# Kernel optimization log

Hardware: AMD Instinct MI355X
Metric: run time of the kernel (lower is better)

Reference implementation:

```python
import jax, jax.numpy as jnp
import numpy as np

N, F, H, R, E = 50000, 128, 128, 8, 800000
BN_EPS = 1e-5


def setup_inputs() -> dict:
    key = jax.random.key(0)
    ks = jax.random.split(key, 10)
    g = lambda k, shp: jax.random.normal(k, shp, dtype=jnp.float32) * (1.0 / np.sqrt(shp[-2] if len(shp) > 1 else shp[-1]))
    return {
        "x": jax.random.normal(ks[0], (N, F), dtype=jnp.float32),
        "edge_index": jax.random.randint(ks[1], (2, E), 0, N, dtype=jnp.int32),
        "edge_type": jax.random.randint(ks[2], (E,), 0, R, dtype=jnp.int32),
        "W1": g(ks[3], (F, H)),
        "b1": jnp.zeros((H,), jnp.float32),
        "weight": g(ks[4], (R, H, H)),
        "root": g(ks[5], (H, H)),
        "bias_c": jnp.zeros((H,), jnp.float32),
        "gamma": jnp.ones((H,), jnp.float32),
        "beta": jnp.zeros((H,), jnp.float32),
        "W2": g(ks[6], (H, H)),
        "b2": jnp.zeros((H,), jnp.float32),
        "Wo": g(ks[7], (H, 1)),
        "bo": jnp.zeros((1,), jnp.float32),
    }


def reference(x, edge_index, edge_type, W1, b1, weight, root, bias_c, gamma, beta, W2, b2, Wo, bo):
    n = x.shape[0]
    r = weight.shape[0]
    src, dst = edge_index[0], edge_index[1]
    # segment id combining relation and destination node: equivalent to the
    # per-relation edge-mask + scatter-add loop in RGCNConv, but in one pass.
    seg = edge_type.astype(jnp.int32) * n + dst

    def conv(h):
        msg = h[src]                                            # [E, H] gather
        agg = jax.ops.segment_sum(msg, seg, num_segments=r * n)  # [R*N, H]
        agg = agg.reshape(r, n, -1)                             # [R, N, H]
        out = jnp.einsum('rnc,rco->no', agg, weight)            # per-relation matmul, summed
        return out + h @ root + bias_c

    def bn(h):
        mu = h.mean(axis=0)
        var = h.var(axis=0)  # biased var, matches torch BN training normalization
        return gamma * (h - mu) * jax.lax.rsqrt(var + BN_EPS) + beta

    h = x @ W1 + b1
    h = jax.nn.relu(bn(conv(h)))
    h = jax.nn.relu(bn(conv(h)))
    h = h @ W2 + b2
    h = h @ Wo + bo
    return jax.nn.sigmoid(h)
```

## Files before the change

kernel.cpp:

```cpp
#include <hip/hip_runtime.h>
#include <stdint.h>

typedef __bf16 bf16;
typedef __bf16 bf16x8 __attribute__((ext_vector_type(8)));
typedef float f32x4 __attribute__((ext_vector_type(4)));

__device__ __forceinline__ float bfbits2f(uint32_t lo16) {
    uint32_t b = lo16 << 16;
    float f;
    __builtin_memcpy(&f, &b, 4);
    return f;
}

__device__ __forceinline__ void gload_lds16(const void* g, void* l) {
    __builtin_amdgcn_global_load_lds((const __attribute__((address_space(1))) void*)g,
                                     (__attribute__((address_space(3))) void*)l, 16, 0, 0);
}

__global__ void k_prep(const float* __restrict__ W1, const float* __restrict__ weight,
                       const float* __restrict__ root, const float* __restrict__ W2,
                       const float* __restrict__ b2, const float* __restrict__ Wo,
                       const float* __restrict__ bo, bf16* __restrict__ W1T,
                       bf16* __restrict__ WhwT, float* __restrict__ qc, int R) {
    int total = 16384 * (R + 2);
    for (int i = blockIdx.x * blockDim.x + threadIdx.x; i < total + 129; i += gridDim.x * blockDim.x) {
        if (i < 16384) {
            int f = i >> 7, h = i & 127;
            W1T[h * 128 + f] = (bf16)W1[f * 128 + h];
        } else if (i < total) {
            int j = i - 16384;
            int r = j >> 14, rem = j & 16383, c = rem >> 7, k = rem & 127;
            float v = (r < R) ? weight[((size_t)(r * 128 + k)) * 128 + c] : root[(size_t)k * 128 + c];
            WhwT[(size_t)(r * 128 + c) * 128 + k] = (bf16)v;
        } else {
            int t = i - total;
            if (t < 128) {
                float s = 0.f;
                for (int j = 0; j < 128; j++) s += W2[t * 128 + j] * Wo[j];
                qc[t] = s;
            } else {
                float c = bo[0];
                for (int j = 0; j < 128; j++) c += b2[j] * Wo[j];
                qc[128] = c;
            }
        }
    }
}

__global__ void k_hist(const int* __restrict__ dst, int* __restrict__ cnt, int E) {
    for (int e = blockIdx.x * blockDim.x + threadIdx.x; e < E; e += gridDim.x * blockDim.x)
        atomicAdd(&cnt[dst[e]], 1);
}

__global__ __launch_bounds__(256) void k_scan_blk(const int* __restrict__ cnt, int* __restrict__ bsum, int N) {
    int i = blockIdx.x * 256 + threadIdx.x;
    int v = (i < N) ? cnt[i] : 0;
#pragma unroll
    for (int d = 1; d < 64; d <<= 1) v += __shfl_xor(v, d);
    __shared__ int ws[4];
    if ((threadIdx.x & 63) == 0) ws[threadIdx.x >> 6] = v;
    __syncthreads();
    if (threadIdx.x == 0) bsum[blockIdx.x] = ws[0] + ws[1] + ws[2] + ws[3];
}

__global__ __launch_bounds__(256) void k_scan_top(int* __restrict__ bsum, int nb) {
    __shared__ int s[256];
    int t = threadIdx.x;
    int v = (t < nb) ? bsum[t] : 0;
    s[t] = v;
    __syncthreads();
#pragma unroll
    for (int d = 1; d < 256; d <<= 1) {
        int u = (t >= d) ? s[t - d] : 0;
        __syncthreads();
        s[t] += u;
        __syncthreads();
    }
    if (t < nb) bsum[t] = s[t] - v;
}

__global__ __launch_bounds__(256) void k_scan_apply(const int* __restrict__ cnt, const int* __restrict__ bsum,
                                                    int* __restrict__ row_off, int* __restrict__ cursor, int N) {
    int b = blockIdx.x, t = threadIdx.x;
    int i = b * 256 + t;
    int v = (i < N) ? cnt[i] : 0;
    int lane = t & 63, wid = t >> 6;
    int incl = v;
#pragma unroll
    for (int d = 1; d < 64; d <<= 1) {
        int u = __shfl_up(incl, d);
        if (lane >= d) incl += u;
    }
    __shared__ int ws[4];
    if (lane == 63) ws[wid] = incl;
    __syncthreads();
    int woff = 0;
    for (int wj = 0; wj < 4; wj++)
        if (wj < wid) woff += ws[wj];
    int excl = bsum[b] + woff + incl - v;
    if (i < N) {
        row_off[i] = excl;
        cursor[i] = excl;
        if (i == N - 1) row_off[N] = excl + v;
    }
}

__global__ void k_fill(const int* __restrict__ src, const int* __restrict__ dst,
                       const int* __restrict__ etype, int* __restrict__ cursor,
                       int* __restrict__ csr, int E, int pbase) {
    int p = blockIdx.x & 7;
    int bg = blockIdx.x >> 3;
    int nchunk = gridDim.x >> 3;
    int chunk = (E + nchunk - 1) / nchunk;
    int beg = bg * chunk, end = min(beg + chunk, E);
    int lo = p * pbase, hi = lo + pbase;
    for (int e = beg + (int)threadIdx.x; e < end; e += blockDim.x) {
        int d = dst[e];
        if (d >= lo && d < hi) {
            int pos = atomicAdd(&cursor[d], 1);
            csr[pos] = (etype[e] << 16) | src[e];
        }
    }
}

__global__ __launch_bounds__(256) void k_gemm0(const float* __restrict__ A, const bf16* __restrict__ BT,
                                               const float* __restrict__ bias, bf16* __restrict__ C, int M) {
    __shared__ bf16 sA[128 * 128];
    __shared__ bf16 sB[128 * 128];
    int tid = threadIdx.x;
    int m0 = blockIdx.x * 128;
#pragma unroll
    for (int i = 0; i < 8; i++) {
        int chunk = i * 256 + tid;
        int row = chunk >> 4, c16 = chunk & 15;
        int sw = ((c16 ^ (row & 7)) << 3);
        int gr = m0 + row;
        int4 va = {0, 0, 0, 0};
        if (gr < M) {
            const float* ap = A + (size_t)gr * 128 + (c16 << 3);
            float4 f0 = *reinterpret_cast<const float4*>(ap);
            float4 f1 = *reinterpret_cast<const float4*>(ap + 4);
            bf16 tmp[8] = {(bf16)f0.x, (bf16)f0.y, (bf16)f0.z, (bf16)f0.w,
                           (bf16)f1.x, (bf16)f1.y, (bf16)f1.z, (bf16)f1.w};
            __builtin_memcpy(&va, tmp, 16);
        }
        *reinterpret_cast<int4*>(&sA[row * 128 + sw]) = va;
        int4 vb = *reinterpret_cast<const int4*>(&BT[(size_t)row * 128 + (c16 << 3)]);
        *reinterpret_cast<int4*>(&sB[row * 128 + sw]) = vb;
    }
    __syncthreads();

    int lane = tid & 63, w = tid >> 6;
    int wm = (w >> 1) * 64, wn = (w & 1) * 64;
    int lr = lane & 15, lk = lane >> 4;
    f32x4 zero = {0.f, 0.f, 0.f, 0.f};
    f32x4 acc[4][4];
#pragma unroll
    for (int mi = 0; mi < 4; mi++)
#pragma unroll
        for (int ni = 0; ni < 4; ni++) acc[mi][ni] = zero;

#pragma unroll
    for (int kk = 0; kk < 4; kk++) {
        int c = (kk << 2) + lk;
        bf16x8 af[4], bfr[4];
#pragma unroll
        for (int mi = 0; mi < 4; mi++) {
            int r = wm + mi * 16 + lr;
            af[mi] = *reinterpret_cast<const bf16x8*>(&sA[r * 128 + ((c ^ (r & 7)) << 3)]);
        }
#pragma unroll
        for (int ni = 0; ni < 4; ni++) {
            int r = wn + ni * 16 + lr;
            bfr[ni] = *reinterpret_cast<const bf16x8*>(&sB[r * 128 + ((c ^ (r & 7)) << 3)]);
        }
#pragma unroll
        for (int mi = 0; mi < 4; mi++)
#pragma unroll
            for (int ni = 0; ni < 4; ni++)
                acc[mi][ni] = __builtin_amdgcn_mfma_f32_16x16x32_bf16(af[mi], bfr[ni], acc[mi][ni], 0, 0, 0);
    }

#pragma unroll
    for (int ni = 0; ni < 4; ni++) {
        int col = wn + ni * 16 + lr;
        float bia = bias[col];
#pragma unroll
        for (int mi = 0; mi < 4; mi++) {
#pragma unroll
            for (int j = 0; j < 4; j++) {
                int row = m0 + wm + mi * 16 + lk * 4 + j;
                if (row < M) C[(size_t)row * 128 + col] = (bf16)(acc[mi][ni][j] + bia);
            }
        }
    }
}

__global__ __launch_bounds__(256) void k_hwgemm(const bf16* __restrict__ h, const bf16* __restrict__ WhwT,
                                                bf16* __restrict__ HW, int M, int NS) {
    __shared__ bf16 sA[128 * 128];
    __shared__ bf16 sB[128 * 128];
    int tid = threadIdx.x;
    int m0 = blockIdx.x * 128;
    int lane = tid & 63, w = tid >> 6;
    int l4 = lane >> 4, c16 = lane & 15;
    int wm = (w >> 1) * 64, wn = (w & 1) * 64;
    int lr = lane & 15, lk = lane >> 4;
    int ldhw = NS * 128;

#pragma unroll
    for (int i = 0; i < 8; i++) {
        int row = i * 16 + (w << 2) + l4;
        int cs = (c16 ^ (row & 7)) << 3;
        int gr = m0 + row;
        gr = gr < M ? gr : M - 1;
        gload_lds16(h + (size_t)gr * 128 + cs, &sA[(i * 256 + (w << 6)) * 8]);
    }
    asm volatile("s_waitcnt vmcnt(0)" ::: "memory");
    __syncthreads();

    bf16x8 af[4][4];
#pragma unroll
    for (int kk = 0; kk < 4; kk++) {
        int c = (kk << 2) + lk;
#pragma unroll
        for (int mi = 0; mi < 4; mi++) {
            int r = wm + mi * 16 + lr;
            af[kk][mi] = *reinterpret_cast<const bf16x8*>(&sA[r * 128 + ((c ^ (r & 7)) << 3)]);
        }
    }
    __syncthreads();

    for (int ns = 0; ns < NS; ns++) {
#pragma unroll
        for (int i = 0; i < 8; i++) {
            int row = i * 16 + (w << 2) + l4;
            int cs = (c16 ^ (row & 7)) << 3;
            gload_lds16(WhwT + (size_t)(ns * 128 + row) * 128 + cs, &sB[(i * 256 + (w << 6)) * 8]);
        }
        asm volatile("s_waitcnt vmcnt(0)" ::: "memory");
        __syncthreads();

        f32x4 zero = {0.f, 0.f, 0.f, 0.f};
        f32x4 acc[4][4];
#pragma unroll
        for (int mi = 0; mi < 4; mi++)
#pragma unroll
            for (int ni = 0; ni < 4; ni++) acc[mi][ni] = zero;

#pragma unroll
        for (int kk = 0; kk < 4; kk++) {
            int c = (kk << 2) + lk;
            bf16x8 bfr[4];
#pragma unroll
            for (int ni = 0; ni < 4; ni++) {
                int r = wn + ni * 16 + lr;
                bfr[ni] = *reinterpret_cast<const bf16x8*>(&sB[r * 128 + ((c ^ (r & 7)) << 3)]);
            }
#pragma unroll
            for (int mi = 0; mi < 4; mi++)
#pragma unroll
                for (int ni = 0; ni < 4; ni++)
                    acc[mi][ni] = __builtin_amdgcn_mfma_f32_16x16x32_bf16(af[kk][mi], bfr[ni], acc[mi][ni], 0, 0, 0);
        }

#pragma unroll
        for (int ni = 0; ni < 4; ni++) {
            int col = ns * 128 + wn + ni * 16 + lr;
#pragma unroll
            for (int mi = 0; mi < 4; mi++) {
#pragma unroll
                for (int j = 0; j < 4; j++) {
                    int row = m0 + wm + mi * 16 + lk * 4 + j;
                    if (row < M) HW[(size_t)row * ldhw + col] = (bf16)acc[mi][ni][j];
                }
            }
        }
        __syncthreads();
    }
}

__global__ __launch_bounds__(128) void k_agg3(const bf16* __restrict__ HW, const int* __restrict__ row_off,
                                              const int* __restrict__ csr, const float* __restrict__ bias,
                                              float* __restrict__ conv, int N, int ldhw, int R) {
    int wi = threadIdx.x >> 6;
    int n = blockIdx.x * 2 + wi;
    if (n >= N) return;
    int lane = threadIdx.x & 63;
    int c0 = lane * 2;
    float a0 = 0.f, a1 = 0.f;
    int beg = row_off[n], end = row_off[n + 1];
    int i = beg;
    for (; i + 4 <= end; i += 4) {
        int p0 = csr[i], p1 = csr[i + 1], p2 = csr[i + 2], p3 = csr[i + 3];
        uint32_t v0 = *reinterpret_cast<const uint32_t*>(&HW[(size_t)(p0 & 0xffff) * ldhw + ((p0 >> 16) << 7) + c0]);
        uint32_t v1 = *reinterpret_cast<const uint32_t*>(&HW[(size_t)(p1 & 0xffff) * ldhw + ((p1 >> 16) << 7) + c0]);
        uint32_t v2 = *reinterpret_cast<const uint32_t*>(&HW[(size_t)(p2 & 0xffff) * ldhw + ((p2 >> 16) << 7) + c0]);
        uint32_t v3 = *reinterpret_cast<const uint32_t*>(&HW[(size_t)(p3 & 0xffff) * ldhw + ((p3 >> 16) << 7) + c0]);
        a0 += bfbits2f(v0 & 0xffffu); a1 += bfbits2f(v0 >> 16);
        a0 += bfbits2f(v1 & 0xffffu); a1 += bfbits2f(v1 >> 16);
        a0 += bfbits2f(v2 & 0xffffu); a1 += bfbits2f(v2 >> 16);
        a0 += bfbits2f(v3 & 0xffffu); a1 += bfbits2f(v3 >> 16);
    }
    for (; i < end; i++) {
        int p = csr[i];
        uint32_t v = *reinterpret_cast<const uint32_t*>(&HW[(size_t)(p & 0xffff) * ldhw + ((p >> 16) << 7) + c0]);
        a0 += bfbits2f(v & 0xffffu); a1 += bfbits2f(v >> 16);
    }
    uint32_t vr = *reinterpret_cast<const uint32_t*>(&HW[(size_t)n * ldhw + (R << 7) + c0]);
    a0 += bfbits2f(vr & 0xffffu) + bias[c0];
    a1 += bfbits2f(vr >> 16) + bias[c0 + 1];
    float2 st = {a0, a1};
    *reinterpret_cast<float2*>(&conv[(size_t)n * 128 + c0]) = st;
}

__global__ __launch_bounds__(256) void k_stats(const float* __restrict__ conv, float* __restrict__ stats, int N) {
    __shared__ float cs[128], cs2[128];
    int tid = threadIdx.x;
    if (tid < 128) { cs[tid] = 0.f; cs2[tid] = 0.f; }
    __syncthreads();
    int c = (tid & 63) * 2;
    int rg = tid >> 6;
    float s0 = 0.f, s20 = 0.f, s1 = 0.f, s21 = 0.f;
    for (int row = blockIdx.x * 4 + rg; row < N; row += gridDim.x * 4) {
        float2 v = *reinterpret_cast<const float2*>(&conv[(size_t)row * 128 + c]);
        s0 += v.x; s20 += v.x * v.x;
        s1 += v.y; s21 += v.y * v.y;
    }
    atomicAdd(&cs[c], s0); atomicAdd(&cs[c + 1], s1);
    atomicAdd(&cs2[c], s20); atomicAdd(&cs2[c + 1], s21);
    __syncthreads();
    if (tid < 128) {
        atomicAdd(&stats[tid], cs[tid]);
        atomicAdd(&stats[128 + tid], cs2[tid]);
    }
}

__global__ void k_bnfin(float* __restrict__ stats, const float* __restrict__ gamma,
                        const float* __restrict__ beta, float* __restrict__ bnp, float invN) {
    int t = threadIdx.x;
    float mu = stats[t] * invN;
    float var = stats[128 + t] * invN - mu * mu;
    float sc = gamma[t] * rsqrtf(var + 1e-5f);
    bnp[t] = sc;
    bnp[128 + t] = beta[t] - mu * sc;
    stats[t] = 0.f;
    stats[128 + t] = 0.f;
}

__global__ void k_bnrelu(const float* __restrict__ conv, const float* __restrict__ bnp,
                         bf16* __restrict__ h, int N) {
    int total = N * 32;
    for (int i = blockIdx.x * blockDim.x + threadIdx.x; i < total; i += gridDim.x * blockDim.x) {
        int c4 = (i & 31) << 2;
        float4 v = *reinterpret_cast<const float4*>(&conv[(size_t)i * 4]);
        const float* vv = &v.x;
        uint64_t pk = 0;
#pragma unroll
        for (int j = 0; j < 4; j++) {
            int c = c4 + j;
            float val = fmaxf(vv[j] * bnp[c] + bnp[128 + c], 0.f);
            unsigned short us = __builtin_bit_cast(unsigned short, (bf16)val);
            pk |= (uint64_t)us << (16 * j);
        }
        *reinterpret_cast<uint64_t*>(&h[(size_t)i * 4]) = pk;
    }
}

__global__ __launch_bounds__(256) void k_bnout(const float* __restrict__ conv, const float* __restrict__ bnp,
                                               const float* __restrict__ qc, float* __restrict__ out, int N) {
    int wi = threadIdx.x >> 6;
    int n = blockIdx.x * 4 + wi;
    if (n >= N) return;
    int lane = threadIdx.x & 63;
    int c0 = lane * 2;
    float2 v = *reinterpret_cast<const float2*>(&conv[(size_t)n * 128 + c0]);
    float v0 = fmaxf(v.x * bnp[c0] + bnp[128 + c0], 0.f);
    float v1 = fmaxf(v.y * bnp[c0 + 1] + bnp[128 + c0 + 1], 0.f);
    float s = v0 * qc[c0] + v1 * qc[c0 + 1];
#pragma unroll
    for (int d = 1; d < 64; d <<= 1) s += __shfl_xor(s, d);
    if (lane == 0) out[n] = 1.f / (1.f + expf(-(s + qc[128])));
}

extern "C" void kernel_launch(void* const* d_in, const int* in_sizes, int n_in,
                              void* d_out, int out_size, void* d_ws, size_t ws_size,
                              hipStream_t stream) {
    const float* x      = (const float*)d_in[0];
    const int*   ei     = (const int*)d_in[1];
    const int*   etype  = (const int*)d_in[2];
    const float* W1     = (const float*)d_in[3];
    const float* b1     = (const float*)d_in[4];
    const float* weight = (const float*)d_in[5];
    const float* root   = (const float*)d_in[6];
    const float* bias_c = (const float*)d_in[7];
    const float* gamma  = (const float*)d_in[8];
    const float* beta   = (const float*)d_in[9];
    const float* W2     = (const float*)d_in[10];
    const float* b2     = (const float*)d_in[11];
    const float* Wo     = (const float*)d_in[12];
    const float* bo     = (const float*)d_in[13];
    float* out = (float*)d_out;

    int H = in_sizes[4];
    int F = in_sizes[3] / H;
    int N = in_sizes[0] / F;
    int E = in_sizes[2];
    int R = in_sizes[5] / (H * H);
    int NS = R + 1;
    int ldhw = NS * H;

    const int* srcv = ei;
    const int* dstv = ei + E;

    char* p = (char*)d_ws;
    auto alloc = [&](size_t bytes) -> char* {
        char* r = p;
        p += (bytes + 255) & ~(size_t)255;
        return r;
    };
    bf16*  HW      = (bf16*)alloc((size_t)N * ldhw * 2);
    bf16*  h       = (bf16*)alloc((size_t)N * H * 2);
    float* conv    = (float*)alloc((size_t)N * H * 4);
    bf16*  WhwT    = (bf16*)alloc((size_t)ldhw * H * 2);
    bf16*  W1T     = (bf16*)alloc((size_t)F * H * 2);
    float* qc      = (float*)alloc(129 * 4);
    int*   cnt     = (int*)alloc((size_t)N * 4);
    int*   row_off = (int*)alloc((size_t)(N + 1) * 4);
    int*   cursor  = (int*)alloc((size_t)N * 4);
    int*   csr     = (int*)alloc((size_t)E * 4);
    float* stats   = (float*)alloc(256 * 4);
    float* bnp     = (float*)alloc(256 * 4);
    int*   bsum    = (int*)alloc(256 * 4);
    if ((size_t)(p - (char*)d_ws) > ws_size) return;

    int nb = (N + 255) / 256;
    int pbase = (N + 7) / 8;

    hipMemsetAsync(cnt, 0, (size_t)N * 4, stream);
    hipMemsetAsync(stats, 0, 256 * 4, stream);
    k_prep<<<256, 256, 0, stream>>>(W1, weight, root, W2, b2, Wo, bo, W1T, WhwT, qc, R);
    k_hist<<<1024, 256, 0, stream>>>(dstv, cnt, E);
    k_scan_blk<<<nb, 256, 0, stream>>>(cnt, bsum, N);
    k_scan_top<<<1, 256, 0, stream>>>(bsum, nb);
    k_scan_apply<<<nb, 256, 0, stream>>>(cnt, bsum, row_off, cursor, N);
    k_fill<<<1024, 256, 0, stream>>>(srcv, dstv, etype, cursor, csr, E, pbase);

    int mb = (N + 127) / 128;
    k_gemm0<<<mb, 256, 0, stream>>>(x, W1T, b1, h, N);

    for (int l = 0; l < 2; l++) {
        k_hwgemm<<<mb, 256, 0, stream>>>(h, WhwT, HW, N, NS);
        k_agg3<<<(N + 1) / 2, 128, 0, stream>>>(HW, row_off, csr, bias_c, conv, N, ldhw, R);
        k_stats<<<512, 256, 0, stream>>>(conv, stats, N);
        k_bnfin<<<1, 128, 0, stream>>>(stats, gamma, beta, bnp, 1.f / (float)N);
        if (l == 0)
            k_bnrelu<<<2048, 256, 0, stream>>>(conv, bnp, h, N);
        else
            k_bnout<<<(N + 3) / 4, 256, 0, stream>>>(conv, bnp, qc, out, N);
    }
}
```

Baseline: 327.6 us.

## Fuse BN statistics into aggregation and load GEMM operands directly from global

Folds the per-channel sum and sum-of-squares reduction into the aggregation kernel, which now runs on a fixed grid of blocks over contiguous node chunks. This removes the separate stats pass that re-read the conv output. The aggregation gather is unrolled to 8 independent loads to expose more memory-level parallelism. The HW GEMM drops its LDS staging and reads A and B fragments straight from global memory, and writes HW with nontemporal stores. This trades LDS traffic and barriers for uncoalesced, cache-dependent global fragment loads.

```diff
diff --git a/kernel.cpp b/kernel.cpp
--- a/kernel.cpp
+++ b/kernel.cpp
@@ -10,11 +10,6 @@
     float f;
     __builtin_memcpy(&f, &b, 4);
     return f;
-}
-
-__device__ __forceinline__ void gload_lds16(const void* g, void* l) {
-    __builtin_amdgcn_global_load_lds((const __attribute__((address_space(1))) void*)g,
-                                     (__attribute__((address_space(3))) void*)l, 16, 0, 0);
 }
 
 __global__ void k_prep(const float* __restrict__ W1, const float* __restrict__ weight,
@@ -198,49 +193,26 @@
 
 __global__ __launch_bounds__(256) void k_hwgemm(const bf16* __restrict__ h, const bf16* __restrict__ WhwT,
                                                 bf16* __restrict__ HW, int M, int NS) {
-    __shared__ bf16 sA[128 * 128];
-    __shared__ bf16 sB[128 * 128];
     int tid = threadIdx.x;
     int m0 = blockIdx.x * 128;
     int lane = tid & 63, w = tid >> 6;
-    int l4 = lane >> 4, c16 = lane & 15;
     int wm = (w >> 1) * 64, wn = (w & 1) * 64;
     int lr = lane & 15, lk = lane >> 4;
     int ldhw = NS * 128;
 
-#pragma unroll
-    for (int i = 0; i < 8; i++) {
-        int row = i * 16 + (w << 2) + l4;
-        int cs = (c16 ^ (row & 7)) << 3;
-        int gr = m0 + row;
-        gr = gr < M ? gr : M - 1;
-        gload_lds16(h + (size_t)gr * 128 + cs, &sA[(i * 256 + (w << 6)) * 8]);
-    }
-    asm volatile("s_waitcnt vmcnt(0)" ::: "memory");
-    __syncthreads();
-
     bf16x8 af[4][4];
 #pragma unroll
     for (int kk = 0; kk < 4; kk++) {
         int c = (kk << 2) + lk;
 #pragma unroll
         for (int mi = 0; mi < 4; mi++) {
-            int r = wm + mi * 16 + lr;
-            af[kk][mi] = *reinterpret_cast<const bf16x8*>(&sA[r * 128 + ((c ^ (r & 7)) << 3)]);
-        }
-    }
-    __syncthreads();
+            int gr = m0 + wm + mi * 16 + lr;
+            gr = gr < M ? gr : M - 1;
+            af[kk][mi] = *reinterpret_cast<const bf16x8*>(&h[(size_t)gr * 128 + (c << 3)]);
+        }
+    }
 
     for (int ns = 0; ns < NS; ns++) {
-#pragma unroll
-        for (int i = 0; i < 8; i++) {
-            int row = i * 16 + (w << 2) + l4;
-            int cs = (c16 ^ (row & 7)) << 3;
-            gload_lds16(WhwT + (size_t)(ns * 128 + row) * 128 + cs, &sB[(i * 256 + (w << 6)) * 8]);
-        }
-        asm volatile("s_waitcnt vmcnt(0)" ::: "memory");
-        __syncthreads();
-
         f32x4 zero = {0.f, 0.f, 0.f, 0.f};
         f32x4 acc[4][4];
 #pragma unroll
@@ -254,8 +226,8 @@
             bf16x8 bfr[4];
 #pragma unroll
             for (int ni = 0; ni < 4; ni++) {
-                int r = wn + ni * 16 + lr;
-                bfr[ni] = *reinterpret_cast<const bf16x8*>(&sB[r * 128 + ((c ^ (r & 7)) << 3)]);
+                int o = ns * 128 + wn + ni * 16 + lr;
+                bfr[ni] = *reinterpret_cast<const bf16x8*>(&WhwT[(size_t)o * 128 + (c << 3)]);
             }
 #pragma unroll
             for (int mi = 0; mi < 4; mi++)
@@ -272,63 +244,66 @@
 #pragma unroll
                 for (int j = 0; j < 4; j++) {
                     int row = m0 + wm + mi * 16 + lk * 4 + j;
-                    if (row < M) HW[(size_t)row * ldhw + col] = (bf16)acc[mi][ni][j];
+                    if (row < M)
+                        __builtin_nontemporal_store((bf16)acc[mi][ni][j], &HW[(size_t)row * ldhw + col]);
                 }
             }
         }
-        __syncthreads();
-    }
-}
-
-__global__ __launch_bounds__(128) void k_agg3(const bf16* __restrict__ HW, const int* __restrict__ row_off,
+    }
+}
+
+__global__ __launch_bounds__(256) void k_agg3(const bf16* __restrict__ HW, const int* __restrict__ row_off,
                                               const int* __restrict__ csr, const float* __restrict__ bias,
-                                              float* __restrict__ conv, int N, int ldhw, int R) {
-    int wi = threadIdx.x >> 6;
-    int n = blockIdx.x * 2 + wi;
-    if (n >= N) return;
-    int lane = threadIdx.x & 63;
-    int c0 = lane * 2;
-    float a0 = 0.f, a1 = 0.f;
-    int beg = row_off[n], end = row_off[n + 1];
-    int i = beg;
-    for (; i + 4 <= end; i += 4) {
-        int p0 = csr[i], p1 = csr[i + 1], p2 = csr[i + 2], p3 = csr[i + 3];
-        uint32_t v0 = *reinterpret_cast<const uint32_t*>(&HW[(size_t)(p0 & 0xffff) * ldhw + ((p0 >> 16) << 7) + c0]);
-        uint32_t v1 = *reinterpret_cast<const uint32_t*>(&HW[(size_t)(p1 & 0xffff) * ldhw + ((p1 >> 16) << 7) + c0]);
-        uint32_t v2 = *reinterpret_cast<const uint32_t*>(&HW[(size_t)(p2 & 0xffff) * ldhw + ((p2 >> 16) << 7) + c0]);
-        uint32_t v3 = *reinterpret_cast<const uint32_t*>(&HW[(size_t)(p3 & 0xffff) * ldhw + ((p3 >> 16) << 7) + c0]);
-        a0 += bfbits2f(v0 & 0xffffu); a1 += bfbits2f(v0 >> 16);
-        a0 += bfbits2f(v1 & 0xffffu); a1 += bfbits2f(v1 >> 16);
-        a0 += bfbits2f(v2 & 0xffffu); a1 += bfbits2f(v2 >> 16);
-        a0 += bfbits2f(v3 & 0xffffu); a1 += bfbits2f(v3 >> 16);
-    }
-    for (; i < end; i++) {
-        int p = csr[i];
-        uint32_t v = *reinterpret_cast<const uint32_t*>(&HW[(size_t)(p & 0xffff) * ldhw + ((p >> 16) << 7) + c0]);
-        a0 += bfbits2f(v & 0xffffu); a1 += bfbits2f(v >> 16);
-    }
-    uint32_t vr = *reinterpret_cast<const uint32_t*>(&HW[(size_t)n * ldhw + (R << 7) + c0]);
-    a0 += bfbits2f(vr & 0xffffu) + bias[c0];
-    a1 += bfbits2f(vr >> 16) + bias[c0 + 1];
-    float2 st = {a0, a1};
-    *reinterpret_cast<float2*>(&conv[(size_t)n * 128 + c0]) = st;
-}
-
-__global__ __launch_bounds__(256) void k_stats(const float* __restrict__ conv, float* __restrict__ stats, int N) {
+                                              float* __restrict__ conv, float* __restrict__ stats,
+                                              int N, int ldhw, int R) {
     __shared__ float cs[128], cs2[128];
     int tid = threadIdx.x;
+    int lane = tid & 63, w = tid >> 6;
     if (tid < 128) { cs[tid] = 0.f; cs2[tid] = 0.f; }
     __syncthreads();
-    int c = (tid & 63) * 2;
-    int rg = tid >> 6;
-    float s0 = 0.f, s20 = 0.f, s1 = 0.f, s21 = 0.f;
-    for (int row = blockIdx.x * 4 + rg; row < N; row += gridDim.x * 4) {
-        float2 v = *reinterpret_cast<const float2*>(&conv[(size_t)row * 128 + c]);
-        s0 += v.x; s20 += v.x * v.x;
-        s1 += v.y; s21 += v.y * v.y;
-    }
-    atomicAdd(&cs[c], s0); atomicAdd(&cs[c + 1], s1);
-    atomicAdd(&cs2[c], s20); atomicAdd(&cs2[c + 1], s21);
+    int c0 = lane * 2;
+    float bia0 = bias[c0], bia1 = bias[c0 + 1];
+    int chunk = (N + gridDim.x - 1) / gridDim.x;
+    int nbeg = blockIdx.x * chunk;
+    int nend = min(nbeg + chunk, N);
+    float st0 = 0.f, st1 = 0.f, st20 = 0.f, st21 = 0.f;
+
+    for (int n = nbeg + w; n < nend; n += 4) {
+        float a0 = 0.f, a1 = 0.f;
+        int beg = row_off[n], end = row_off[n + 1];
+        int i = beg;
+        for (; i + 8 <= end; i += 8) {
+            int pp[8];
+            uint32_t vv[8];
+#pragma unroll
+            for (int u = 0; u < 8; u++) pp[u] = csr[i + u];
+#pragma unroll
+            for (int u = 0; u < 8; u++)
+                vv[u] = *reinterpret_cast<const uint32_t*>(
+                    &HW[(size_t)(pp[u] & 0xffff) * ldhw + (((uint32_t)pp[u] >> 16) << 7) + c0]);
+#pragma unroll
+            for (int u = 0; u < 8; u++) {
+                a0 += bfbits2f(vv[u] & 0xffffu);
+                a1 += bfbits2f(vv[u] >> 16);
+            }
+        }
+        for (; i < end; i++) {
+            int p = csr[i];
+            uint32_t v = *reinterpret_cast<const uint32_t*>(
+                &HW[(size_t)(p & 0xffff) * ldhw + (((uint32_t)p >> 16) << 7) + c0]);
+            a0 += bfbits2f(v & 0xffffu);
+            a1 += bfbits2f(v >> 16);
+        }
+        uint32_t vr = *reinterpret_cast<const uint32_t*>(&HW[(size_t)n * ldhw + (R << 7) + c0]);
+        a0 += bfbits2f(vr & 0xffffu) + bia0;
+        a1 += bfbits2f(vr >> 16) + bia1;
+        float2 st = {a0, a1};
+        *reinterpret_cast<float2*>(&conv[(size_t)n * 128 + c0]) = st;
+        st0 += a0; st20 += a0 * a0;
+        st1 += a1; st21 += a1 * a1;
+    }
+    atomicAdd(&cs[c0], st0); atomicAdd(&cs[c0 + 1], st1);
+    atomicAdd(&cs2[c0], st20); atomicAdd(&cs2[c0 + 1], st21);
     __syncthreads();
     if (tid < 128) {
         atomicAdd(&stats[tid], cs[tid]);
@@ -451,8 +426,7 @@
 
     for (int l = 0; l < 2; l++) {
         k_hwgemm<<<mb, 256, 0, stream>>>(h, WhwT, HW, N, NS);
-        k_agg3<<<(N + 1) / 2, 128, 0, stream>>>(HW, row_off, csr, bias_c, conv, N, ldhw, R);
-        k_stats<<<512, 256, 0, stream>>>(conv, stats, N);
+        k_agg3<<<1024, 256, 0, stream>>>(HW, row_off, csr, bias_c, conv, stats, N, ldhw, R);
         k_bnfin<<<1, 128, 0, stream>>>(stats, gamma, beta, bnp, 1.f / (float)N);
         if (l == 0)
             k_bnrelu<<<2048, 256, 0, stream>>>(conv, bnp, h, N);
```

Measured after the change: 569.1 us. 1.74x slower.
